# Performance work log

Hardware: AMD Instinct MI355X
Metric: run time of the kernel (lower is better)

Reference implementation:

```python
import jax, jax.numpy as jnp
import numpy as np

B, SQ, SK, D, H, HD = 2, 2048, 2048, 1024, 16, 64


def setup_inputs() -> dict:
    key = jax.random.key(0)
    ks = jax.random.split(key, 10)
    s = 1.0 / np.sqrt(D)  # keep activations well-scaled
    return {
        "x": jax.random.normal(ks[0], (B, SQ, D), jnp.float32),
        "encoder_output": jax.random.normal(ks[1], (B, SK, D), jnp.float32),
        "Wq": jax.random.normal(ks[2], (H, D, HD), jnp.float32) * s,
        "bq": jax.random.normal(ks[3], (H, HD), jnp.float32) * 0.01,
        "Wk": jax.random.normal(ks[4], (H, D, HD), jnp.float32) * s,
        "bk": jax.random.normal(ks[5], (H, HD), jnp.float32) * 0.01,
        "Wv": jax.random.normal(ks[6], (H, D, HD), jnp.float32) * s,
        "bv": jax.random.normal(ks[7], (H, HD), jnp.float32) * 0.01,
        "Wo": jax.random.normal(ks[8], (D, D), jnp.float32) * s,
        "bo": jax.random.normal(ks[9], (D,), jnp.float32) * 0.01,
    }


def reference(x, encoder_output, Wq, bq, Wk, bk, Wv, bv, Wo, bo):
    # Batched per-head projections (equivalent to the per-head nn.Linear loop).
    q = jnp.einsum('bsd,hde->bhse', x, Wq) + bq[None, :, None, :]              # [B,H,SQ,HD]
    k = jnp.einsum('bsd,hde->bhse', encoder_output, Wk) + bk[None, :, None, :]  # [B,H,SK,HD]
    v = jnp.einsum('bsd,hde->bhse', encoder_output, Wv) + bv[None, :, None, :]  # [B,H,SK,HD]
    scale = 1.0 / jnp.sqrt(jnp.asarray(HD, q.dtype))
    scores = jnp.einsum('bhqe,bhke->bhqk', q, k) * scale                        # [B,H,SQ,SK]
    attn = jax.nn.softmax(scores, axis=-1)
    out = jnp.einsum('bhqk,bhke->bhqe', attn, v)                                # [B,H,SQ,HD]
    # concat heads along feature dim (head order matches torch.cat order)
    out = out.transpose(0, 2, 1, 3).reshape(out.shape[0], out.shape[2], -1)     # [B,SQ,D]
    # final linear; dropout is identity in eval mode
    return out @ Wo + bo
```

## Files before the change

### kernel.cpp

```cpp
#include <hip/hip_runtime.h>


typedef unsigned short u16;
typedef __bf16 bf16x8 __attribute__((ext_vector_type(8)));
typedef float f32x4 __attribute__((ext_vector_type(4)));
typedef float f32x16 __attribute__((ext_vector_type(16)));
typedef unsigned u32x2 __attribute__((ext_vector_type(2)));

#define B_ 2
#define SQ_ 2048
#define SK_ 2048
#define D_ 1024
#define H_ 16
#define HD_ 64

__device__ __forceinline__ u16 f2bf(float f) {
  union { float f; unsigned u; } c; c.f = f;
  unsigned u = c.u;
  return (u16)((u + 0x7fffu + ((u >> 16) & 1u)) >> 16);
}
__device__ __forceinline__ float bf2f(u16 h) {
  union { unsigned u; float f; } c; c.u = ((unsigned)h) << 16;
  return c.f;
}
__device__ __forceinline__ unsigned pack_bf16(float lo, float hi) {
  union { __bf16 h[2]; unsigned u; } c;
  c.h[0] = (__bf16)lo;
  c.h[1] = (__bf16)hi;
  return c.u;
}

#define GLOAD_LDS16(gp, lp)                                                  \
  __builtin_amdgcn_global_load_lds(                                          \
      (const __attribute__((address_space(1))) void*)(gp),                   \
      (__attribute__((address_space(3))) void*)(lp), 16, 0, 0)

__global__ __launch_bounds__(256) void cast2_f32_bf16(const float* __restrict__ x,
                                                      const float* __restrict__ enc,
                                                      u16* __restrict__ xb,
                                                      u16* __restrict__ eb) {
  const float* in = blockIdx.z ? enc : x;
  u16* out = blockIdx.z ? eb : xb;
  int i = blockIdx.x * 256 + threadIdx.x;
  float4 v = ((const float4*)in)[i];
  uint2 p;
  p.x = (unsigned)f2bf(v.x) | ((unsigned)f2bf(v.y) << 16);
  p.y = (unsigned)f2bf(v.z) | ((unsigned)f2bf(v.w) << 16);
  ((uint2*)out)[i] = p;
}

__global__ __launch_bounds__(256) void wqkv_trans(const float* __restrict__ Wq,
                                                  const float* __restrict__ Wk,
                                                  const float* __restrict__ Wv,
                                                  u16* __restrict__ out) {
  __shared__ float tile[64][65];
  const int mat = blockIdx.z >> 4, head = blockIdx.z & 15;
  const float* W = (mat == 0) ? Wq : (mat == 1 ? Wk : Wv);
  const float* ib = W + (long)head * 65536;
  u16* ob = out + ((long)mat << 20) + (long)head * 65536;
  int r0 = blockIdx.y << 6;
  int tid = threadIdx.x;
#pragma unroll
  for (int i = 0; i < 16; ++i) {
    int idx = tid + (i << 8);
    int r = idx >> 6, c = idx & 63;
    tile[r][c] = ib[(long)(r0 + r) * 64 + c];
  }
  __syncthreads();
#pragma unroll
  for (int i = 0; i < 16; ++i) {
    int idx = tid + (i << 8);
    int cc = idx >> 6, rr = idx & 63;
    ob[(long)cc * 1024 + (r0 + rr)] = f2bf(tile[rr][cc]);
  }
}

__global__ __launch_bounds__(256) void transpose_to_bf16(const float* __restrict__ in,
                                                         u16* __restrict__ out,
                                                         int R, int C,
                                                         long ibs, long obs) {
  __shared__ float tile[64][65];
  const float* ib = in + (long)blockIdx.z * ibs;
  u16* ob = out + (long)blockIdx.z * obs;
  int r0 = blockIdx.y << 6, c0 = blockIdx.x << 6;
  int tid = threadIdx.x;
#pragma unroll
  for (int i = 0; i < 16; ++i) {
    int idx = tid + (i << 8);
    int r = idx >> 6, c = idx & 63;
    tile[r][c] = ib[(long)(r0 + r) * C + (c0 + c)];
  }
  __syncthreads();
#pragma unroll
  for (int i = 0; i < 16; ++i) {
    int idx = tid + (i << 8);
    int cc = idx >> 6, rr = idx & 63;
    ob[(long)(c0 + cc) * R + (r0 + rr)] = f2bf(tile[rr][cc]);
  }
}

__global__ __launch_bounds__(256) void gemm_qkv(const u16* __restrict__ xb,
                                                const u16* __restrict__ eb,
                                                const u16* __restrict__ Wt3,
                                                const float* __restrict__ bq,
                                                const float* __restrict__ bk,
                                                const float* __restrict__ bv,
                                                u16* __restrict__ qws,
                                                u16* __restrict__ kws,
                                                u16* __restrict__ vT) {
  constexpr int M = 2048, N = 1024, K = 1024;
  __shared__ __align__(16) u16 As[128 * 32];
  __shared__ __align__(16) u16 Bs[128 * 32];
  const int tid = threadIdx.x;
  const int lane = tid & 63;
  const int wid = tid >> 6;
  const int l16 = lane & 15, quad = lane >> 4;
  const int wm = wid >> 1, wn = wid & 1;
  const int bn0g = blockIdx.x << 7;
  const int seg = bn0g >> 10;
  const int bn0 = bn0g & (N - 1);
  const int bm0 = blockIdx.y << 7;
  const u16* A = (seg == 0) ? xb : eb;
  const u16* Wt = Wt3 + ((long)seg << 20);
  const float* bias = (seg == 0) ? bq : (seg == 1 ? bk : bv);
  const long abase = (long)blockIdx.z * M * K;

  f32x4 acc[4][4];
#pragma unroll
  for (int i = 0; i < 4; ++i)
#pragma unroll
    for (int j = 0; j < 4; ++j) acc[i][j] = f32x4{0.f, 0.f, 0.f, 0.f};

  const int r0 = tid >> 2;
  const int c0s = (tid & 3) << 3;
  const u16* agp = A + abase + (long)(bm0 + r0) * K + c0s;
  const u16* bgp = Wt + (long)(bn0 + r0) * K + c0s;
  u16* alp = As + tid * 8;
  u16* blp = Bs + tid * 8;

  for (int k0 = 0; k0 < K; k0 += 32) {
    GLOAD_LDS16(agp + k0, alp);
    GLOAD_LDS16(agp + k0 + (long)64 * K, alp + 2048);
    GLOAD_LDS16(bgp + k0, blp);
    GLOAD_LDS16(bgp + k0 + (long)64 * K, blp + 2048);
    __syncthreads();
    bf16x8 af[4], bfr[4];
#pragma unroll
    for (int mi = 0; mi < 4; ++mi)
      af[mi] = *(const bf16x8*)(As + (wm * 64 + mi * 16 + l16) * 32 + quad * 8);
#pragma unroll
    for (int ni = 0; ni < 4; ++ni)
      bfr[ni] = *(const bf16x8*)(Bs + (wn * 64 + ni * 16 + l16) * 32 + quad * 8);
#pragma unroll
    for (int mi = 0; mi < 4; ++mi)
#pragma unroll
      for (int ni = 0; ni < 4; ++ni)
        acc[mi][ni] = __builtin_amdgcn_mfma_f32_16x16x32_bf16(af[mi], bfr[ni],
                                                              acc[mi][ni], 0, 0, 0);
    __syncthreads();
  }

  float bv4[4];
#pragma unroll
  for (int ni = 0; ni < 4; ++ni) bv4[ni] = bias[bn0 + wn * 64 + ni * 16 + l16];

  if (seg == 2) {
    const long zb = (long)blockIdx.z * N * M;
#pragma unroll
    for (int mi = 0; mi < 4; ++mi)
#pragma unroll
      for (int ni = 0; ni < 4; ++ni) {
        int colg = bn0 + wn * 64 + ni * 16 + l16;
        int rowg = bm0 + wm * 64 + mi * 16 + (quad << 2);
        ushort4 pk = make_ushort4(f2bf(acc[mi][ni][0] + bv4[ni]),
                                  f2bf(acc[mi][ni][1] + bv4[ni]),
                                  f2bf(acc[mi][ni][2] + bv4[ni]),
                                  f2bf(acc[mi][ni][3] + bv4[ni]));
        *(ushort4*)(vT + zb + (long)colg * M + rowg) = pk;
      }
  } else {
    u16* outp = seg ? kws : qws;
    const long cbase = (long)blockIdx.z * M * N;
#pragma unroll
    for (int mi = 0; mi < 4; ++mi)
#pragma unroll
      for (int ni = 0; ni < 4; ++ni)
#pragma unroll
        for (int r = 0; r < 4; ++r) {
          int row = bm0 + wm * 64 + mi * 16 + (quad << 2) + r;
          int col = bn0 + wn * 64 + ni * 16 + l16;
          outp[cbase + (long)row * N + col] = f2bf(acc[mi][ni][r] + bv4[ni]);
        }
  }
}

__global__ __launch_bounds__(256) void gemm_final(const u16* __restrict__ A,
                                                  const u16* __restrict__ Wt,
                                                  const float* __restrict__ bias,
                                                  float* __restrict__ C) {
  constexpr int M = 2048, N = 1024, K = 1024;
  __shared__ __align__(16) u16 As[64 * 32];
  __shared__ __align__(16) u16 Bs[128 * 32];
  const int tid = threadIdx.x;
  const int lane = tid & 63;
  const int wid = tid >> 6;
  const int l16 = lane & 15, quad = lane >> 4;
  const int bn0 = blockIdx.x << 7, bm0 = blockIdx.y << 6;

  f32x4 acc[4][2];
#pragma unroll
  for (int i = 0; i < 4; ++i)
#pragma unroll
    for (int j = 0; j < 2; ++j) acc[i][j] = f32x4{0.f, 0.f, 0.f, 0.f};

  const int r0 = tid >> 2;
  const int c0s = (tid & 3) << 3;
  const long abase = (long)blockIdx.z * M * K;
  const u16* agp = A + abase + (long)(bm0 + r0) * K + c0s;
  const u16* bgp = Wt + (long)(bn0 + r0) * K + c0s;
  u16* alp = As + tid * 8;
  u16* blp = Bs + tid * 8;

  for (int k0 = 0; k0 < K; k0 += 32) {
    GLOAD_LDS16(agp + k0, alp);
    GLOAD_LDS16(bgp + k0, blp);
    GLOAD_LDS16(bgp + k0 + (long)64 * K, blp + 2048);
    __syncthreads();
    bf16x8 af[4], bfr[2];
#pragma unroll
    for (int mi = 0; mi < 4; ++mi)
      af[mi] = *(const bf16x8*)(As + (mi * 16 + l16) * 32 + quad * 8);
#pragma unroll
    for (int ni = 0; ni < 2; ++ni)
      bfr[ni] = *(const bf16x8*)(Bs + (wid * 32 + ni * 16 + l16) * 32 + quad * 8);
#pragma unroll
    for (int mi = 0; mi < 4; ++mi)
#pragma unroll
      for (int ni = 0; ni < 2; ++ni)
        acc[mi][ni] = __builtin_amdgcn_mfma_f32_16x16x32_bf16(af[mi], bfr[ni],
                                                              acc[mi][ni], 0, 0, 0);
    __syncthreads();
  }

  float bv2[2];
#pragma unroll
  for (int ni = 0; ni < 2; ++ni) bv2[ni] = bias[bn0 + wid * 32 + ni * 16 + l16];
  const long cbase = (long)blockIdx.z * M * N;
#pragma unroll
  for (int mi = 0; mi < 4; ++mi)
#pragma unroll
    for (int ni = 0; ni < 2; ++ni)
#pragma unroll
      for (int r = 0; r < 4; ++r) {
        int row = bm0 + mi * 16 + (quad << 2) + r;
        int col = bn0 + wid * 32 + ni * 16 + l16;
        C[cbase + (long)row * N + col] = acc[mi][ni][r] + bv2[ni];
      }
}


#define ATTN_STAGE(kbase, vbase)                                              \
  do {                                                                        \
    GLOAD_LDS16(kp, (kbase) + tid * 8);                                       \
    GLOAD_LDS16(kp + (long)32 * D_, (kbase) + 2048 + tid * 8);                \
    GLOAD_LDS16(vp, (vbase) + tid * 8);                                       \
    GLOAD_LDS16(vp + (long)32 * SK_, (vbase) + 2048 + tid * 8);               \
    kp += (long)64 * D_;                                                      \
    vp += 64;                                                                 \
  } while (0)

#define QK_BLOCK(Kb, sx0, sx1)                                                \
  do {                                                                        \
    _Pragma("unroll") for (int i = 0; i < 16; ++i) { sx0[i] = 0.f; sx1[i] = 0.f; } \
    _Pragma("unroll") for (int j = 0; j < 4; ++j) {                           \
      bf16x8 kf0 = *(const bf16x8*)((Kb) + ro0 + sw[j]);                      \
      bf16x8 kf1 = *(const bf16x8*)((Kb) + 2048 + ro0 + sw[j]);               \
      sx0 = __builtin_amdgcn_mfma_f32_32x32x16_bf16(kf0, qf[j], sx0, 0, 0, 0);\
      sx1 = __builtin_amdgcn_mfma_f32_32x32x16_bf16(kf1, qf[j], sx1, 0, 0, 0);\
    }                                                                         \
  } while (0)

#define EXPD(sx0, sx1)                                                        \
  do {                                                                        \
    _Pragma("unroll") for (int g = 0; g < 8; ++g) {                           \
      float a0 = __expf(sx0[2 * g]);                                          \
      float a1 = __expf(sx0[2 * g + 1]);                                      \
      float b0 = __expf(sx1[2 * g]);                                          \
      float b1 = __expf(sx1[2 * g + 1]);                                      \
      psA += a0 + a1;                                                         \
      psB += b0 + b1;                                                         \
      d0[g] = pack_bf16(a0, a1);                                              \
      d1[g] = pack_bf16(b0, b1);                                              \
    }                                                                         \
  } while (0)

#define PV_KS(Vb, dd, k1, ks)                                                 \
  do {                                                                        \
    u32x2 sA = __builtin_amdgcn_permlane32_swap(dd[4 * (k1)],                 \
                                                dd[4 * (k1) + 2], false,      \
                                                false);                       \
    u32x2 sB = __builtin_amdgcn_permlane32_swap(dd[4 * (k1) + 1],             \
                                                dd[4 * (k1) + 3], false,      \
                                                false);                       \
    union { unsigned u[4]; bf16x8 v; } pa;                                    \
    pa.u[0] = sA[0]; pa.u[1] = sB[0]; pa.u[2] = sA[1]; pa.u[3] = sB[1];       \
    bf16x8 v0 = *(const bf16x8*)((Vb) + ro0 + sw[ks]);                        \
    bf16x8 v1 = *(const bf16x8*)((Vb) + 2048 + ro0 + sw[ks]);                 \
    o0 = __builtin_amdgcn_mfma_f32_32x32x16_bf16(pa.v, v0, o0, 0, 0, 0);      \
    o1 = __builtin_amdgcn_mfma_f32_32x32x16_bf16(pa.v, v1, o1, 0, 0, 0);      \
  } while (0)

#define PV4(Vb)                                                               \
  do {                                                                        \
    PV_KS(Vb, d0, 0, 0);                                                      \
    PV_KS(Vb, d0, 1, 1);                                                      \
    PV_KS(Vb, d1, 0, 2);                                                      \
    PV_KS(Vb, d1, 1, 3);                                                      \
  } while (0)

__global__ __launch_bounds__(256, 2) void attn_flash(const u16* __restrict__ q,
                                                     const u16* __restrict__ k,
                                                     const u16* __restrict__ vT,
                                                     u16* __restrict__ ctx) {
  __shared__ __align__(16) u16 Ks[2 * 4096];
  __shared__ __align__(16) u16 Vs[3 * 4096];

  const int tid = threadIdx.x;
  const int lane = tid & 63;
  const int wid = tid >> 6;
  const int l31 = lane & 31, h5 = lane >> 5;
  const int h = blockIdx.y, b = blockIdx.z;
  const int q0w = (blockIdx.x << 7) + (wid << 5);

  bf16x8 qf[4];
  const u16* qp = q + ((long)(b * SQ_ + q0w + l31) * D_ + h * HD_ + 8 * h5);
#pragma unroll
  for (int j = 0; j < 4; ++j) {
    bf16x8 t = *(const bf16x8*)(qp + 16 * j);
#pragma unroll
    for (int e = 0; e < 8; ++e) t[e] = (__bf16)((float)t[e] * 0.125f);
    qf[j] = t;
  }

  const int srow = tid >> 3;
  const int ssw = ((tid & 7) ^ (srow & 7)) << 3;
  const u16* kp = k + ((long)(b * SK_ + srow) * D_ + h * HD_ + ssw);
  const u16* vp = vT + ((long)(b * D_ + h * HD_ + srow) * SK_ + ssw);

  const int ro0 = l31 << 6;
  int sw[4];
#pragma unroll
  for (int i = 0; i < 4; ++i) sw[i] = ((2 * i + h5) ^ (lane & 7)) << 3;

  f32x16 o0, o1, sA0, sA1, sB0, sB1;
#pragma unroll
  for (int i = 0; i < 16; ++i) { o0[i] = 0.f; o1[i] = 0.f; }
  float psA = 0.f, psB = 0.f;
  unsigned d0[8], d1[8];

  ATTN_STAGE(Ks, Vs);
  ATTN_STAGE(Ks + 4096, Vs + 4096);
  __syncthreads();
  QK_BLOCK(Ks, sA0, sA1);

  int viP = 0;
  int viS = 2;

  for (int tp = 0; tp < 30; tp += 2) {
    __syncthreads();
    ATTN_STAGE(Ks, Vs + viS * 4096);
    viS = (viS == 2) ? 0 : viS + 1;
    QK_BLOCK(Ks + 4096, sB0, sB1);
    EXPD(sA0, sA1);
    PV4(Vs + viP * 4096);
    viP = (viP == 2) ? 0 : viP + 1;
    __syncthreads();
    ATTN_STAGE(Ks + 4096, Vs + viS * 4096);
    viS = (viS == 2) ? 0 : viS + 1;
    QK_BLOCK(Ks, sA0, sA1);
    EXPD(sB0, sB1);
    PV4(Vs + viP * 4096);
    viP = (viP == 2) ? 0 : viP + 1;
  }
  __syncthreads();
  QK_BLOCK(Ks + 4096, sB0, sB1);
  EXPD(sA0, sA1);
  PV4(Vs + viP * 4096);
  viP = (viP == 2) ? 0 : viP + 1;
  __syncthreads();
  EXPD(sB0, sB1);
  PV4(Vs + viP * 4096);

  float ps = psA + psB;
  ps += __shfl_xor(ps, 32, 64);
  float inv = 1.f / ps;

#pragma unroll
  for (int r = 0; r < 16; ++r) {
    const int crow = (r & 3) + 8 * (r >> 2) + 4 * h5;
    float dq = __shfl(inv, crow, 64);
    long base = (long)(b * SQ_ + q0w + crow) * D_ + h * HD_ + l31;
    ctx[base] = f2bf(o0[r] * dq);
    ctx[base + 32] = f2bf(o1[r] * dq);
  }
}

extern "C" void kernel_launch(void* const* d_in, const int* in_sizes, int n_in,
                              void* d_out, int out_size, void* d_ws, size_t ws_size,
                              hipStream_t stream) {
  const float* x   = (const float*)d_in[0];
  const float* enc = (const float*)d_in[1];
  const float* Wq  = (const float*)d_in[2];
  const float* bq  = (const float*)d_in[3];
  const float* Wk  = (const float*)d_in[4];
  const float* bk  = (const float*)d_in[5];
  const float* Wv  = (const float*)d_in[6];
  const float* bv  = (const float*)d_in[7];
  const float* Wo  = (const float*)d_in[8];
  const float* bo  = (const float*)d_in[9];

  const long NE_X = (long)B_ * SQ_ * D_;
  const long NE_W = (long)D_ * D_;

  u16* outA = (u16*)d_out;
  u16* outB = outA + NE_X;
  u16* eb  = outB;
  u16* vTp = outA;

  u16* ws  = (u16*)d_ws;
  u16* WqT = ws;
  u16* WoT = WqT + 3 * NE_W;
  u16* qws = WoT + NE_W;
  u16* kws = qws + NE_X;
  u16* xb  = kws + NE_X;
  u16* ctx = xb;

  cast2_f32_bf16<<<dim3((unsigned)(NE_X / 4 / 256), 1, 2), 256, 0, stream>>>(x, enc, xb, eb);

  wqkv_trans<<<dim3(1, 16, 48), 256, 0, stream>>>(Wq, Wk, Wv, WqT);
  transpose_to_bf16<<<dim3(16, 16, 1), 256, 0, stream>>>(Wo, WoT, 1024, 1024, 0L, 0L);

  gemm_qkv<<<dim3(24, 16, 2), 256, 0, stream>>>(xb, eb, WqT, bq, bk, bv,
                                                qws, kws, vTp);

  attn_flash<<<dim3(SQ_ / 128, H_, B_), 256, 0, stream>>>(qws, kws, vTp, ctx);

  gemm_final<<<dim3(8, 32, 2), 256, 0, stream>>>(ctx, WoT, bo, (float*)d_out);
}
```

Baseline: 228.5 us.

## Fuse prep kernels, deepen GEMM K-tiles to 64 with swizzled LDS, seed QK MFMA with zero

Merges the three preprocessing kernels (activation cast, QKV weight transpose, Wo transpose) into one launch that dispatches on block index, removing two launch gaps. Both GEMMs now stage 64-wide K tiles per barrier pair instead of 32, using an XOR swizzle on the LDS column index to avoid bank conflicts. This halves the number of barriers. The attention QK block now starts its first MFMA from a zero vector instead of clearing accumulators in a loop. The larger tiles double the GEMMs' LDS use, which may reduce occupancy.

```diff
diff --git a/kernel.cpp b/kernel.cpp
--- a/kernel.cpp
+++ b/kernel.cpp
@@ -35,67 +35,72 @@
       (const __attribute__((address_space(1))) void*)(gp),                   \
       (__attribute__((address_space(3))) void*)(lp), 16, 0, 0)
 
-__global__ __launch_bounds__(256) void cast2_f32_bf16(const float* __restrict__ x,
-                                                      const float* __restrict__ enc,
-                                                      u16* __restrict__ xb,
-                                                      u16* __restrict__ eb) {
-  const float* in = blockIdx.z ? enc : x;
-  u16* out = blockIdx.z ? eb : xb;
-  int i = blockIdx.x * 256 + threadIdx.x;
-  float4 v = ((const float4*)in)[i];
-  uint2 p;
-  p.x = (unsigned)f2bf(v.x) | ((unsigned)f2bf(v.y) << 16);
-  p.y = (unsigned)f2bf(v.z) | ((unsigned)f2bf(v.w) << 16);
-  ((uint2*)out)[i] = p;
-}
-
-__global__ __launch_bounds__(256) void wqkv_trans(const float* __restrict__ Wq,
+__global__ __launch_bounds__(256) void prep_fused(const float* __restrict__ x,
+                                                  const float* __restrict__ enc,
+                                                  const float* __restrict__ Wq,
                                                   const float* __restrict__ Wk,
                                                   const float* __restrict__ Wv,
-                                                  u16* __restrict__ out) {
+                                                  const float* __restrict__ Wo,
+                                                  u16* __restrict__ xb,
+                                                  u16* __restrict__ eb,
+                                                  u16* __restrict__ WqT,
+                                                  u16* __restrict__ WoT) {
   __shared__ float tile[64][65];
-  const int mat = blockIdx.z >> 4, head = blockIdx.z & 15;
-  const float* W = (mat == 0) ? Wq : (mat == 1 ? Wk : Wv);
-  const float* ib = W + (long)head * 65536;
-  u16* ob = out + ((long)mat << 20) + (long)head * 65536;
-  int r0 = blockIdx.y << 6;
-  int tid = threadIdx.x;
-#pragma unroll
-  for (int i = 0; i < 16; ++i) {
-    int idx = tid + (i << 8);
-    int r = idx >> 6, c = idx & 63;
-    tile[r][c] = ib[(long)(r0 + r) * 64 + c];
-  }
-  __syncthreads();
-#pragma unroll
-  for (int i = 0; i < 16; ++i) {
-    int idx = tid + (i << 8);
-    int cc = idx >> 6, rr = idx & 63;
-    ob[(long)cc * 1024 + (r0 + rr)] = f2bf(tile[rr][cc]);
-  }
-}
-
-__global__ __launch_bounds__(256) void transpose_to_bf16(const float* __restrict__ in,
-                                                         u16* __restrict__ out,
-                                                         int R, int C,
-                                                         long ibs, long obs) {
-  __shared__ float tile[64][65];
-  const float* ib = in + (long)blockIdx.z * ibs;
-  u16* ob = out + (long)blockIdx.z * obs;
-  int r0 = blockIdx.y << 6, c0 = blockIdx.x << 6;
-  int tid = threadIdx.x;
-#pragma unroll
-  for (int i = 0; i < 16; ++i) {
-    int idx = tid + (i << 8);
-    int r = idx >> 6, c = idx & 63;
-    tile[r][c] = ib[(long)(r0 + r) * C + (c0 + c)];
-  }
-  __syncthreads();
-#pragma unroll
-  for (int i = 0; i < 16; ++i) {
-    int idx = tid + (i << 8);
-    int cc = idx >> 6, rr = idx & 63;
-    ob[(long)(c0 + cc) * R + (r0 + rr)] = f2bf(tile[rr][cc]);
+  const int id = blockIdx.x;
+  const int tid = threadIdx.x;
+
+  if (id < 8192) {
+    const float* in = (id >= 4096) ? enc : x;
+    u16* out = (id >= 4096) ? eb : xb;
+    int i = (id & 4095) * 256 + tid;
+    float4 v = ((const float4*)in)[i];
+    uint2 p;
+    p.x = (unsigned)f2bf(v.x) | ((unsigned)f2bf(v.y) << 16);
+    p.y = (unsigned)f2bf(v.z) | ((unsigned)f2bf(v.w) << 16);
+    ((uint2*)out)[i] = p;
+    return;
+  }
+
+  if (id < 8960) {
+    const int f = id - 8192;
+    const int z48 = f >> 4, y = f & 15;
+    const int mat = z48 >> 4, head = z48 & 15;
+    const float* W = (mat == 0) ? Wq : (mat == 1 ? Wk : Wv);
+    const float* ib = W + (long)head * 65536;
+    u16* ob = WqT + ((long)mat << 20) + (long)head * 65536;
+    const int r0 = y << 6;
+#pragma unroll
+    for (int i = 0; i < 16; ++i) {
+      int idx = tid + (i << 8);
+      int r = idx >> 6, c = idx & 63;
+      tile[r][c] = ib[(long)(r0 + r) * 64 + c];
+    }
+    __syncthreads();
+#pragma unroll
+    for (int i = 0; i < 16; ++i) {
+      int idx = tid + (i << 8);
+      int cc = idx >> 6, rr = idx & 63;
+      ob[(long)cc * 1024 + (r0 + rr)] = f2bf(tile[rr][cc]);
+    }
+    return;
+  }
+
+  {
+    const int g = id - 8960;
+    const int c0 = (g & 15) << 6, r0 = (g >> 4) << 6;
+#pragma unroll
+    for (int i = 0; i < 16; ++i) {
+      int idx = tid + (i << 8);
+      int r = idx >> 6, c = idx & 63;
+      tile[r][c] = Wo[(long)(r0 + r) * 1024 + (c0 + c)];
+    }
+    __syncthreads();
+#pragma unroll
+    for (int i = 0; i < 16; ++i) {
+      int idx = tid + (i << 8);
+      int cc = idx >> 6, rr = idx & 63;
+      WoT[(long)(c0 + cc) * 1024 + (r0 + rr)] = f2bf(tile[rr][cc]);
+    }
   }
 }
 
@@ -109,8 +114,8 @@
                                                 u16* __restrict__ kws,
                                                 u16* __restrict__ vT) {
   constexpr int M = 2048, N = 1024, K = 1024;
-  __shared__ __align__(16) u16 As[128 * 32];
-  __shared__ __align__(16) u16 Bs[128 * 32];
+  __shared__ __align__(16) u16 As[128 * 64];
+  __shared__ __align__(16) u16 Bs[128 * 64];
   const int tid = threadIdx.x;
   const int lane = tid & 63;
   const int wid = tid >> 6;
@@ -131,32 +136,37 @@
 #pragma unroll
     for (int j = 0; j < 4; ++j) acc[i][j] = f32x4{0.f, 0.f, 0.f, 0.f};
 
-  const int r0 = tid >> 2;
-  const int c0s = (tid & 3) << 3;
+  const int r0 = tid >> 3;
+  const int c0s = ((tid & 7) ^ (r0 & 7)) << 3;
   const u16* agp = A + abase + (long)(bm0 + r0) * K + c0s;
   const u16* bgp = Wt + (long)(bn0 + r0) * K + c0s;
   u16* alp = As + tid * 8;
   u16* blp = Bs + tid * 8;
 
-  for (int k0 = 0; k0 < K; k0 += 32) {
-    GLOAD_LDS16(agp + k0, alp);
-    GLOAD_LDS16(agp + k0 + (long)64 * K, alp + 2048);
-    GLOAD_LDS16(bgp + k0, blp);
-    GLOAD_LDS16(bgp + k0 + (long)64 * K, blp + 2048);
-    __syncthreads();
-    bf16x8 af[4], bfr[4];
-#pragma unroll
-    for (int mi = 0; mi < 4; ++mi)
-      af[mi] = *(const bf16x8*)(As + (wm * 64 + mi * 16 + l16) * 32 + quad * 8);
-#pragma unroll
-    for (int ni = 0; ni < 4; ++ni)
-      bfr[ni] = *(const bf16x8*)(Bs + (wn * 64 + ni * 16 + l16) * 32 + quad * 8);
-#pragma unroll
-    for (int mi = 0; mi < 4; ++mi)
+  for (int k0 = 0; k0 < K; k0 += 64) {
+#pragma unroll
+    for (int i = 0; i < 4; ++i) {
+      GLOAD_LDS16(agp + k0 + (long)(32 * i) * K, alp + i * 2048);
+      GLOAD_LDS16(bgp + k0 + (long)(32 * i) * K, blp + i * 2048);
+    }
+    __syncthreads();
+#pragma unroll
+    for (int kk = 0; kk < 2; ++kk) {
+      const int csw = ((quad + 4 * kk) ^ (l16 & 7)) << 3;
+      bf16x8 af[4], bfr[4];
+#pragma unroll
+      for (int mi = 0; mi < 4; ++mi)
+        af[mi] = *(const bf16x8*)(As + (wm * 64 + mi * 16 + l16) * 64 + csw);
 #pragma unroll
       for (int ni = 0; ni < 4; ++ni)
-        acc[mi][ni] = __builtin_amdgcn_mfma_f32_16x16x32_bf16(af[mi], bfr[ni],
-                                                              acc[mi][ni], 0, 0, 0);
+        bfr[ni] = *(const bf16x8*)(Bs + (wn * 64 + ni * 16 + l16) * 64 + csw);
+#pragma unroll
+      for (int mi = 0; mi < 4; ++mi)
+#pragma unroll
+        for (int ni = 0; ni < 4; ++ni)
+          acc[mi][ni] = __builtin_amdgcn_mfma_f32_16x16x32_bf16(af[mi], bfr[ni],
+                                                                acc[mi][ni], 0, 0, 0);
+    }
     __syncthreads();
   }
 
@@ -199,8 +209,8 @@
                                                   const float* __restrict__ bias,
                                                   float* __restrict__ C) {
   constexpr int M = 2048, N = 1024, K = 1024;
-  __shared__ __align__(16) u16 As[64 * 32];
-  __shared__ __align__(16) u16 Bs[128 * 32];
+  __shared__ __align__(16) u16 As[64 * 64];
+  __shared__ __align__(16) u16 Bs[128 * 64];
   const int tid = threadIdx.x;
   const int lane = tid & 63;
   const int wid = tid >> 6;
@@ -213,32 +223,39 @@
 #pragma unroll
     for (int j = 0; j < 2; ++j) acc[i][j] = f32x4{0.f, 0.f, 0.f, 0.f};
 
-  const int r0 = tid >> 2;
-  const int c0s = (tid & 3) << 3;
+  const int r0 = tid >> 3;
+  const int c0s = ((tid & 7) ^ (r0 & 7)) << 3;
   const long abase = (long)blockIdx.z * M * K;
   const u16* agp = A + abase + (long)(bm0 + r0) * K + c0s;
   const u16* bgp = Wt + (long)(bn0 + r0) * K + c0s;
   u16* alp = As + tid * 8;
   u16* blp = Bs + tid * 8;
 
-  for (int k0 = 0; k0 < K; k0 += 32) {
-    GLOAD_LDS16(agp + k0, alp);
-    GLOAD_LDS16(bgp + k0, blp);
-    GLOAD_LDS16(bgp + k0 + (long)64 * K, blp + 2048);
-    __syncthreads();
-    bf16x8 af[4], bfr[2];
-#pragma unroll
-    for (int mi = 0; mi < 4; ++mi)
-      af[mi] = *(const bf16x8*)(As + (mi * 16 + l16) * 32 + quad * 8);
-#pragma unroll
-    for (int ni = 0; ni < 2; ++ni)
-      bfr[ni] = *(const bf16x8*)(Bs + (wid * 32 + ni * 16 + l16) * 32 + quad * 8);
-#pragma unroll
-    for (int mi = 0; mi < 4; ++mi)
+  for (int k0 = 0; k0 < K; k0 += 64) {
+#pragma unroll
+    for (int i = 0; i < 2; ++i)
+      GLOAD_LDS16(agp + k0 + (long)(32 * i) * K, alp + i * 2048);
+#pragma unroll
+    for (int i = 0; i < 4; ++i)
+      GLOAD_LDS16(bgp + k0 + (long)(32 * i) * K, blp + i * 2048);
+    __syncthreads();
+#pragma unroll
+    for (int kk = 0; kk < 2; ++kk) {
+      const int csw = ((quad + 4 * kk) ^ (l16 & 7)) << 3;
+      bf16x8 af[4], bfr[2];
+#pragma unroll
+      for (int mi = 0; mi < 4; ++mi)
+        af[mi] = *(const bf16x8*)(As + (mi * 16 + l16) * 64 + csw);
 #pragma unroll
       for (int ni = 0; ni < 2; ++ni)
-        acc[mi][ni] = __builtin_amdgcn_mfma_f32_16x16x32_bf16(af[mi], bfr[ni],
-                                                              acc[mi][ni], 0, 0, 0);
+        bfr[ni] = *(const bf16x8*)(Bs + (wid * 32 + ni * 16 + l16) * 64 + csw);
+#pragma unroll
+      for (int mi = 0; mi < 4; ++mi)
+#pragma unroll
+        for (int ni = 0; ni < 2; ++ni)
+          acc[mi][ni] = __builtin_amdgcn_mfma_f32_16x16x32_bf16(af[mi], bfr[ni],
+                                                                acc[mi][ni], 0, 0, 0);
+    }
     __syncthreads();
   }
 
@@ -257,7 +274,6 @@
         C[cbase + (long)row * N + col] = acc[mi][ni][r] + bv2[ni];
       }
 }
-
 
 #define ATTN_STAGE(kbase, vbase)                                              \
   do {                                                                        \
@@ -271,8 +287,13 @@
 
 #define QK_BLOCK(Kb, sx0, sx1)                                                \
   do {                                                                        \
-    _Pragma("unroll") for (int i = 0; i < 16; ++i) { sx0[i] = 0.f; sx1[i] = 0.f; } \
-    _Pragma("unroll") for (int j = 0; j < 4; ++j) {                           \
+    {                                                                         \
+      bf16x8 kf0 = *(const bf16x8*)((Kb) + ro0 + sw[0]);                      \
+      bf16x8 kf1 = *(const bf16x8*)((Kb) + 2048 + ro0 + sw[0]);               \
+      sx0 = __builtin_amdgcn_mfma_f32_32x32x16_bf16(kf0, qf[0], ZV, 0, 0, 0); \
+      sx1 = __builtin_amdgcn_mfma_f32_32x32x16_bf16(kf1, qf[0], ZV, 0, 0, 0); \
+    }                                                                         \
+    _Pragma("unroll") for (int j = 1; j < 4; ++j) {                           \
       bf16x8 kf0 = *(const bf16x8*)((Kb) + ro0 + sw[j]);                      \
       bf16x8 kf1 = *(const bf16x8*)((Kb) + 2048 + ro0 + sw[j]);               \
       sx0 = __builtin_amdgcn_mfma_f32_32x32x16_bf16(kf0, qf[j], sx0, 0, 0, 0);\
@@ -353,6 +374,7 @@
   for (int i = 0; i < 4; ++i) sw[i] = ((2 * i + h5) ^ (lane & 7)) << 3;
 
   f32x16 o0, o1, sA0, sA1, sB0, sB1;
+  f32x16 ZV = {};
 #pragma unroll
   for (int i = 0; i < 16; ++i) { o0[i] = 0.f; o1[i] = 0.f; }
   float psA = 0.f, psB = 0.f;
@@ -374,6 +396,7 @@
     EXPD(sA0, sA1);
     PV4(Vs + viP * 4096);
     viP = (viP == 2) ? 0 : viP + 1;
+
     __syncthreads();
     ATTN_STAGE(Ks + 4096, Vs + viS * 4096);
     viS = (viS == 2) ? 0 : viS + 1;
@@ -435,10 +458,8 @@
   u16* xb  = kws + NE_X;
   u16* ctx = xb;
 
-  cast2_f32_bf16<<<dim3((unsigned)(NE_X / 4 / 256), 1, 2), 256, 0, stream>>>(x, enc, xb, eb);
-
-  wqkv_trans<<<dim3(1, 16, 48), 256, 0, stream>>>(Wq, Wk, Wv, WqT);
-  transpose_to_bf16<<<dim3(16, 16, 1), 256, 0, stream>>>(Wo, WoT, 1024, 1024, 0L, 0L);
+  prep_fused<<<dim3(9216, 1, 1), 256, 0, stream>>>(x, enc, Wq, Wk, Wv, Wo,
+                                                   xb, eb, WqT, WoT);
 
   gemm_qkv<<<dim3(24, 16, 2), 256, 0, stream>>>(xb, eb, WqT, bq, bk, bv,
                                                 qws, kws, vTp);
```

New measurement: 207.1 us. 1.1x faster.
